# Kernel optimization log

Hardware: AMD Instinct MI355X
Metric: run time of the kernel (lower is better)

## Reference

```python
import jax, jax.numpy as jnp
from jax import lax
import numpy as np

NPOINT, RADIUS, NSAMPLE = 2048, 0.2, 32
EPS = 1e-5


def fps(xyz, npoint):
    # furthest point sampling; xyz [B,N,3] -> idx [B,npoint] int32
    B, N, _ = xyz.shape

    def body(carry, _):
        dist, far = carry  # dist [B,N], far [B]
        centroid = jnp.take_along_axis(xyz, far[:, None, None], axis=1)  # [B,1,3]
        d = jnp.sum((xyz - centroid) ** 2, -1)  # [B,N]
        dist = jnp.minimum(dist, d)
        nxt = jnp.argmax(dist, -1).astype(jnp.int32)
        return (dist, nxt), far

    init = (jnp.full((B, N), 1e10, xyz.dtype), jnp.zeros((B,), jnp.int32))
    _, idx = lax.scan(body, init, None, length=npoint)
    return jnp.transpose(idx)  # [B, npoint]


def ball_query(radius, nsample, xyz, new_xyz):
    # xyz [B,N,3], new_xyz [B,S,3] -> idx [B,S,nsample] int32
    B, N, _ = xyz.shape
    sqr = jnp.sum((new_xyz[:, :, None, :] - xyz[:, None, :, :]) ** 2, -1)  # [B,S,N]
    idx = jnp.broadcast_to(jnp.arange(N, dtype=jnp.int32), sqr.shape)
    idx = jnp.where(sqr > radius * radius, N, idx)
    idx = jnp.sort(idx, -1)[:, :, :nsample]  # first nsample in-ball indices
    first = idx[:, :, :1]
    return jnp.where(idx == N, first, idx)  # pad misses with first hit


def group(x, idx):
    # x [B,N,C], idx [B,S,K] -> [B,S,K,C]
    return jax.vmap(lambda xb, ib: xb[ib])(x, idx)


def setup_inputs() -> dict:
    key = jax.random.key(0)
    ks = jax.random.split(key, 8)
    B, N = 8, 8192
    mlp, in_c = [32, 32, 64], 6
    inp = {
        'xyz': jax.random.normal(ks[0], (B, N, 3), jnp.float32),
        'points': jax.random.normal(ks[1], (B, N, 3), jnp.float32),
    }
    cin = in_c
    for i, cout in enumerate(mlp):
        inp[f'w{i}'] = jax.random.normal(ks[2 + i], (cout, cin), jnp.float32) * (1.0 / np.sqrt(cin))
        inp[f'b{i}'] = jnp.zeros((cout,), jnp.float32)
        inp[f'g{i}'] = jnp.ones((cout,), jnp.float32)
        inp[f'be{i}'] = jnp.zeros((cout,), jnp.float32)
        cin = cout
    return inp


def reference(xyz, points, w0, b0, g0, be0, w1, b1, g1, be1, w2, b2, g2, be2):
    fps_idx = fps(xyz, NPOINT)
    new_xyz = jax.vmap(lambda xb, ib: xb[ib])(xyz, fps_idx)  # [B,S,3]
    idx = ball_query(RADIUS, NSAMPLE, xyz, new_xyz)  # [B,S,K]
    grouped_xyz = group(xyz, idx) - new_xyz[:, :, None, :]  # [B,S,K,3]
    feat = jnp.concatenate([grouped_xyz, group(points, idx)], -1)  # [B,S,K,6]
    for w, b, g, be in ((w0, b0, g0, be0), (w1, b1, g1, be1), (w2, b2, g2, be2)):
        feat = jnp.einsum('bskc,oc->bsko', feat, w) + b  # 1x1 conv
        mean = jnp.mean(feat, axis=(0, 1, 2))
        var = jnp.var(feat, axis=(0, 1, 2))
        feat = (feat - mean) * lax.rsqrt(var + EPS) * g + be  # BN (train stats)
        feat = jax.nn.relu(feat)
    new_points = jnp.max(feat, axis=2)  # max over neighborhood -> [B,S,64]
    return new_xyz, new_points
```

## Files before the change

### kernel.cpp

```cpp
#include <hip/hip_runtime.h>
#include <math.h>

#define BB 8
#define NN 8192
#define SS 2048
#define KK 32
#define NP (BB*SS*KK)
#define EPSF 1e-5f

typedef float v2f __attribute__((ext_vector_type(2)));

template <int CTRL>
__device__ __forceinline__ unsigned long long dpp_max_step(unsigned long long key) {
    unsigned lo = (unsigned)key, hi = (unsigned)(key >> 32);
    unsigned nlo = (unsigned)__builtin_amdgcn_update_dpp((int)lo, (int)lo, CTRL, 0xf, 0xf, false);
    unsigned nhi = (unsigned)__builtin_amdgcn_update_dpp((int)hi, (int)hi, CTRL, 0xf, 0xf, false);
    unsigned long long nk = ((unsigned long long)nhi << 32) | nlo;
    return nk > key ? nk : key;
}

__device__ __forceinline__ unsigned long long wave_max_u64(unsigned long long key) {
    key = dpp_max_step<0x111>(key);
    key = dpp_max_step<0x112>(key);
    key = dpp_max_step<0x114>(key);
    key = dpp_max_step<0x118>(key);
    key = dpp_max_step<0x142>(key);
    key = dpp_max_step<0x143>(key);
    return key;
}

__global__ __launch_bounds__(512) void fps_kernel(const float* __restrict__ xyz,
                                                  float* __restrict__ out_newxyz) {
#pragma clang fp contract(off)
    const int T = 512;
    const int NPAIR = 8;
    int b = blockIdx.x;
    int t = threadIdx.x;
    int wid  = t >> 6;
    int lane = t & 63;
    const float* x = xyz + b * NN * 3;
    float* nout = out_newxyz + b * SS * 3;

    __shared__ float4 lxyz[NN];
    __shared__ unsigned long long skey[2][8];

    v2f px2[NPAIR], py2[NPAIR], pz2[NPAIR], d2[NPAIR];
#pragma unroll
    for (int j = 0; j < NPAIR; j++) {
        int p0 = t + (2 * j) * T;
        int p1 = p0 + T;
        float ax = x[p0 * 3 + 0], ay = x[p0 * 3 + 1], az = x[p0 * 3 + 2];
        float bx = x[p1 * 3 + 0], by = x[p1 * 3 + 1], bz = x[p1 * 3 + 2];
        px2[j].x = ax; px2[j].y = bx;
        py2[j].x = ay; py2[j].y = by;
        pz2[j].x = az; pz2[j].y = bz;
        lxyz[p0] = make_float4(ax, ay, az, 0.f);
        lxyz[p1] = make_float4(bx, by, bz, 0.f);
        d2[j].x = 1e10f; d2[j].y = 1e10f;
    }
    __syncthreads();
    float4 c0 = lxyz[0];
    float cx = c0.x, cy = c0.y, cz = c0.z;

    for (int it = 0; it < SS; it++) {
        if (t == 0) {
            nout[it * 3 + 0] = cx;
            nout[it * 3 + 1] = cy;
            nout[it * 3 + 2] = cz;
        }
        v2f cxx, cyy, czz;
        cxx.x = cx; cxx.y = cx;
        cyy.x = cy; cyy.y = cy;
        czz.x = cz; czz.y = cz;
        float lmax = -1.0f;
        int   li   = 0;
#pragma unroll
        for (int j = 0; j < NPAIR; j++) {
            v2f dx = px2[j] - cxx;
            v2f dy = py2[j] - cyy;
            v2f dz = pz2[j] - czz;
            v2f sx = dx * dx;
            v2f sy = dy * dy;
            v2f sz = dz * dz;
            v2f ss = (sx + sy) + sz;
            float e0 = fminf(d2[j].x, ss.x);
            float e1 = fminf(d2[j].y, ss.y);
            d2[j].x = e0;
            d2[j].y = e1;
            bool g0 = e0 > lmax;
            lmax = g0 ? e0 : lmax;
            li   = g0 ? (2 * j) : li;
            bool g1 = e1 > lmax;
            lmax = g1 ? e1 : lmax;
            li   = g1 ? (2 * j + 1) : li;
        }
        int p = t + (li << 9);
        unsigned long long key =
            ((unsigned long long)__float_as_uint(lmax) << 32) | (unsigned)(~p);
        key = wave_max_u64(key);
        if (lane == 63) skey[it & 1][wid] = key;
        __syncthreads();
        unsigned long long k = skey[it & 1][0];
#pragma unroll
        for (int j = 1; j < 8; j++) {
            unsigned long long o = skey[it & 1][j];
            k = (o > k) ? o : k;
        }
        int gi = (int)(~(unsigned)k) & (NN - 1);
        float4 c = lxyz[gi];
        cx = c.x; cy = c.y; cz = c.z;
    }
}

__global__ __launch_bounds__(256) void ballq_kernel(const float* __restrict__ xyz,
                                                    const float* __restrict__ new_xyz,
                                                    int* __restrict__ idx_out) {
    int q    = blockIdx.x * 4 + (threadIdx.x >> 6);
    int lane = threadIdx.x & 63;
    int b    = q >> 11;
    const float* x = xyz + b * NN * 3;
    const float* c = new_xyz + q * 3;
    float cx = c[0], cy = c[1], cz = c[2];
    int* out = idx_out + q * KK;
    const float R2 = (float)(0.2 * 0.2);

    int count = 0;
    int first = -1;
    for (int base = 0; base < NN; base += 64) {
        int p = base + lane;
        float dx = __fsub_rn(x[p * 3 + 0], cx);
        float dy = __fsub_rn(x[p * 3 + 1], cy);
        float dz = __fsub_rn(x[p * 3 + 2], cz);
        float d  = __fadd_rn(__fadd_rn(__fmul_rn(dx, dx), __fmul_rn(dy, dy)),
                             __fmul_rn(dz, dz));
        bool in = !(d > R2);
        unsigned long long m = __ballot(in);
        if (first < 0 && m != 0ull) first = base + __ffsll((unsigned long long)m) - 1;
        int pre = __popcll(m & ((1ull << lane) - 1ull));
        int pos = count + pre;
        if (in && pos < KK) out[pos] = p;
        count += __popcll(m);
        if (count >= KK) break;
    }
    for (int i2 = count + lane; i2 < KK; i2 += 64) out[i2] = first;
}

__device__ __forceinline__ void load_in6(const float* __restrict__ xyz,
                                         const float* __restrict__ points,
                                         const float* __restrict__ new_xyz,
                                         const int* __restrict__ idx, int p, float inx[6]) {
    int bs = p >> 5;
    int b  = bs >> 11;
    int pt = idx[p];
    const float* xb = xyz + ((long)b * NN + pt) * 3;
    const float* pb = points + ((long)b * NN + pt) * 3;
    const float* nx = new_xyz + bs * 3;
    inx[0] = xb[0] - nx[0];
    inx[1] = xb[1] - nx[1];
    inx[2] = xb[2] - nx[2];
    inx[3] = pb[0];
    inx[4] = pb[1];
    inx[5] = pb[2];
}

template <int CIN, int COUT>
__device__ __forceinline__ void linear(const float* __restrict__ w,
                                       const float* __restrict__ bias,
                                       const float* xin, float* yout) {
#pragma unroll
    for (int o = 0; o < COUT; o++) {
        float acc = bias[o];
#pragma unroll
        for (int j = 0; j < CIN; j++) acc = fmaf(w[o * CIN + j], xin[j], acc);
        yout[o] = acc;
    }
}

template <int C>
__device__ __forceinline__ void bn_coef(const float* __restrict__ stats,
                                        const float* __restrict__ g,
                                        const float* __restrict__ be,
                                        float* s_sc, float* s_sh) {
    int t = threadIdx.x;
    if (t < C) {
        float mean = stats[t] * (1.0f / (float)NP);
        float var  = stats[C + t] * (1.0f / (float)NP) - mean * mean;
        float rstd = 1.0f / sqrtf(var + EPSF);
        float sc = g[t] * rstd;
        s_sc[t] = sc;
        s_sh[t] = be[t] - mean * sc;
    }
    __syncthreads();
}

template <int C>
__device__ __forceinline__ void accum_stats(const float* y, float* __restrict__ gstats) {
    __shared__ float buf[256][33];
    int t = threadIdx.x;
#pragma unroll
    for (int h = 0; h < C / 32; h++) {
        __syncthreads();
#pragma unroll
        for (int c = 0; c < 32; c++) buf[t][c] = y[h * 32 + c];
        __syncthreads();
        if (t < 32) {
            float s = 0.f, sq = 0.f;
            for (int r = 0; r < 256; r++) {
                float v = buf[r][t];
                s += v;
                sq = fmaf(v, v, sq);
            }
            atomicAdd(&gstats[h * 32 + t], s);
            atomicAdd(&gstats[C + h * 32 + t], sq);
        }
    }
}

__global__ __launch_bounds__(256) void l0_stats_kernel(
    const float* __restrict__ xyz, const float* __restrict__ points,
    const float* __restrict__ new_xyz, const int* __restrict__ idx,
    const float* __restrict__ w0, const float* __restrict__ b0_,
    float* __restrict__ stats0) {
    int p = blockIdx.x * 256 + threadIdx.x;
    float inx[6];
    load_in6(xyz, points, new_xyz, idx, p, inx);
    float y0[32];
    linear<6, 32>(w0, b0_, inx, y0);
    accum_stats<32>(y0, stats0);
}

__global__ __launch_bounds__(256) void l1_stats_kernel(
    const float* __restrict__ xyz, const float* __restrict__ points,
    const float* __restrict__ new_xyz, const int* __restrict__ idx,
    const float* __restrict__ w0, const float* __restrict__ b0_,
    const float* __restrict__ g0, const float* __restrict__ be0,
    const float* __restrict__ w1, const float* __restrict__ b1_,
    const float* __restrict__ stats0, float* __restrict__ stats1) {
    __shared__ float sc0[32], sh0[32];
    bn_coef<32>(stats0, g0, be0, sc0, sh0);
    int p = blockIdx.x * 256 + threadIdx.x;
    float inx[6];
    load_in6(xyz, points, new_xyz, idx, p, inx);
    float y0[32];
    linear<6, 32>(w0, b0_, inx, y0);
#pragma unroll
    for (int c = 0; c < 32; c++) y0[c] = fmaxf(fmaf(y0[c], sc0[c], sh0[c]), 0.f);
    float y1[32];
    linear<32, 32>(w1, b1_, y0, y1);
    accum_stats<32>(y1, stats1);
}

__global__ __launch_bounds__(256) void l2_stats_kernel(
    const float* __restrict__ xyz, const float* __restrict__ points,
    const float* __restrict__ new_xyz, const int* __restrict__ idx,
    const float* __restrict__ w0, const float* __restrict__ b0_,
    const float* __restrict__ g0, const float* __restrict__ be0,
    const float* __restrict__ w1, const float* __restrict__ b1_,
    const float* __restrict__ g1, const float* __restrict__ be1,
    const float* __restrict__ w2, const float* __restrict__ b2_,
    const float* __restrict__ stats0, const float* __restrict__ stats1,
    float* __restrict__ stats2) {
    __shared__ float sc0[32], sh0[32], sc1[32], sh1[32];
    bn_coef<32>(stats0, g0, be0, sc0, sh0);
    bn_coef<32>(stats1, g1, be1, sc1, sh1);
    int p = blockIdx.x * 256 + threadIdx.x;
    float inx[6];
    load_in6(xyz, points, new_xyz, idx, p, inx);
    float y0[32];
    linear<6, 32>(w0, b0_, inx, y0);
#pragma unroll
    for (int c = 0; c < 32; c++) y0[c] = fmaxf(fmaf(y0[c], sc0[c], sh0[c]), 0.f);
    float y1[32];
    linear<32, 32>(w1, b1_, y0, y1);
#pragma unroll
    for (int c = 0; c < 32; c++) y1[c] = fmaxf(fmaf(y1[c], sc1[c], sh1[c]), 0.f);
    float y2[64];
    linear<32, 64>(w2, b2_, y1, y2);
    accum_stats<64>(y2, stats2);
}

__global__ __launch_bounds__(256) void final_kernel(
    const float* __restrict__ xyz, const float* __restrict__ points,
    const float* __restrict__ new_xyz, const int* __restrict__ idx,
    const float* __restrict__ w0, const float* __restrict__ b0_,
    const float* __restrict__ g0, const float* __restrict__ be0,
    const float* __restrict__ w1, const float* __restrict__ b1_,
    const float* __restrict__ g1, const float* __restrict__ be1,
    const float* __restrict__ w2, const float* __restrict__ b2_,
    const float* __restrict__ g2, const float* __restrict__ be2,
    const float* __restrict__ stats0, const float* __restrict__ stats1,
    const float* __restrict__ stats2, float* __restrict__ out_points) {
    __shared__ float sc0[32], sh0[32], sc1[32], sh1[32], sc2[64], sh2[64];
    bn_coef<32>(stats0, g0, be0, sc0, sh0);
    bn_coef<32>(stats1, g1, be1, sc1, sh1);
    bn_coef<64>(stats2, g2, be2, sc2, sh2);
    int p = blockIdx.x * 256 + threadIdx.x;
    float inx[6];
    load_in6(xyz, points, new_xyz, idx, p, inx);
    float y0[32];
    linear<6, 32>(w0, b0_, inx, y0);
#pragma unroll
    for (int c = 0; c < 32; c++) y0[c] = fmaxf(fmaf(y0[c], sc0[c], sh0[c]), 0.f);
    float y1[32];
    linear<32, 32>(w1, b1_, y0, y1);
#pragma unroll
    for (int c = 0; c < 32; c++) y1[c] = fmaxf(fmaf(y1[c], sc1[c], sh1[c]), 0.f);
    float y2[64];
    linear<32, 64>(w2, b2_, y1, y2);
#pragma unroll
    for (int c = 0; c < 64; c++) {
        float v = fmaxf(fmaf(y2[c], sc2[c], sh2[c]), 0.f);
#pragma unroll
        for (int off = 1; off < 32; off <<= 1)
            v = fmaxf(v, __shfl_xor(v, off));
        y2[c] = v;
    }
    int lane = threadIdx.x & 63;
    if ((lane & 31) == 0) {
        int bs = p >> 5;
        float4* o = (float4*)(out_points + (long)bs * 64);
#pragma unroll
        for (int c4 = 0; c4 < 16; c4++)
            o[c4] = make_float4(y2[c4 * 4], y2[c4 * 4 + 1], y2[c4 * 4 + 2], y2[c4 * 4 + 3]);
    }
}

extern "C" void kernel_launch(void* const* d_in, const int* in_sizes, int n_in,
                              void* d_out, int out_size, void* d_ws, size_t ws_size,
                              hipStream_t stream) {
    (void)in_sizes; (void)n_in; (void)out_size; (void)ws_size;
    const float* xyz    = (const float*)d_in[0];
    const float* points = (const float*)d_in[1];
    const float* w0  = (const float*)d_in[2];
    const float* b0_ = (const float*)d_in[3];
    const float* g0  = (const float*)d_in[4];
    const float* be0 = (const float*)d_in[5];
    const float* w1  = (const float*)d_in[6];
    const float* b1_ = (const float*)d_in[7];
    const float* g1  = (const float*)d_in[8];
    const float* be1 = (const float*)d_in[9];
    const float* w2  = (const float*)d_in[10];
    const float* b2_ = (const float*)d_in[11];
    const float* g2  = (const float*)d_in[12];
    const float* be2 = (const float*)d_in[13];

    float* out        = (float*)d_out;
    float* out_newxyz = out;
    float* out_points = out + BB * SS * 3;

    int*   idx    = (int*)d_ws;
    float* stats  = (float*)d_ws + NP;
    float* stats0 = stats;
    float* stats1 = stats + 64;
    float* stats2 = stats + 128;

    hipMemsetAsync(stats, 0, 256 * sizeof(float), stream);

    fps_kernel<<<BB, 512, 0, stream>>>(xyz, out_newxyz);
    ballq_kernel<<<BB * SS / 4, 256, 0, stream>>>(xyz, out_newxyz, idx);
    l0_stats_kernel<<<NP / 256, 256, 0, stream>>>(xyz, points, out_newxyz, idx, w0, b0_, stats0);
    l1_stats_kernel<<<NP / 256, 256, 0, stream>>>(xyz, points, out_newxyz, idx,
                                                  w0, b0_, g0, be0, w1, b1_, stats0, stats1);
    l2_stats_kernel<<<NP / 256, 256, 0, stream>>>(xyz, points, out_newxyz, idx,
                                                  w0, b0_, g0, be0, w1, b1_, g1, be1,
                                                  w2, b2_, stats0, stats1, stats2);
    final_kernel<<<NP / 256, 256, 0, stream>>>(xyz, points, out_newxyz, idx,
                                               w0, b0_, g0, be0, w1, b1_, g1, be1,
                                               w2, b2_, g2, be2, stats0, stats1, stats2,
                                               out_points);
}
```

Baseline: 2.346 ms.

## Split FPS per batch across four cooperating blocks with global-memory argmax exchange

Furthest point sampling now uses four blocks per batch instead of one, each owning a quarter of the points. Every iteration the blocks publish their local max key to global memory, spin on per-block sequence counters, and then reduce the four keys. The aim is to use more CUs for the serial FPS loop, which previously ran on only 8 blocks. The cost is a cross-block global-memory handshake on each of the 2048 iterations, which adds latency and needs a cooperative launch to guarantee co-residency.

```diff
diff --git a/kernel.cpp b/kernel.cpp
--- a/kernel.cpp
+++ b/kernel.cpp
@@ -7,6 +7,7 @@
 #define KK 32
 #define NP (BB*SS*KK)
 #define EPSF 1e-5f
+#define FG 4
 
 typedef float v2f __attribute__((ext_vector_type(2)));
 
@@ -30,40 +31,50 @@
 }
 
 __global__ __launch_bounds__(512) void fps_kernel(const float* __restrict__ xyz,
-                                                  float* __restrict__ out_newxyz) {
+                                                  float* __restrict__ out_newxyz,
+                                                  unsigned long long* __restrict__ comm,
+                                                  unsigned* __restrict__ seqp) {
 #pragma clang fp contract(off)
     const int T = 512;
-    const int NPAIR = 8;
-    int b = blockIdx.x;
+    const int NPAIR = 2;
+    int blk = blockIdx.x;
+    int b = blk >> 2;
+    int g = blk & (FG - 1);
     int t = threadIdx.x;
     int wid  = t >> 6;
     int lane = t & 63;
     const float* x = xyz + b * NN * 3;
     float* nout = out_newxyz + b * SS * 3;
+    int base = g * (NN / FG);
+    int slot = b * FG + g;
 
     __shared__ float4 lxyz[NN];
     __shared__ unsigned long long skey[2][8];
+    __shared__ unsigned long long gkey[2][FG];
+
+#pragma unroll
+    for (int i = 0; i < NN / T; i++) {
+        int p = t + i * T;
+        lxyz[p] = make_float4(x[p * 3 + 0], x[p * 3 + 1], x[p * 3 + 2], 0.f);
+    }
+    __syncthreads();
 
     v2f px2[NPAIR], py2[NPAIR], pz2[NPAIR], d2[NPAIR];
 #pragma unroll
     for (int j = 0; j < NPAIR; j++) {
-        int p0 = t + (2 * j) * T;
+        int p0 = base + t + (2 * j) * T;
         int p1 = p0 + T;
-        float ax = x[p0 * 3 + 0], ay = x[p0 * 3 + 1], az = x[p0 * 3 + 2];
-        float bx = x[p1 * 3 + 0], by = x[p1 * 3 + 1], bz = x[p1 * 3 + 2];
-        px2[j].x = ax; px2[j].y = bx;
-        py2[j].x = ay; py2[j].y = by;
-        pz2[j].x = az; pz2[j].y = bz;
-        lxyz[p0] = make_float4(ax, ay, az, 0.f);
-        lxyz[p1] = make_float4(bx, by, bz, 0.f);
+        float4 a = lxyz[p0], c = lxyz[p1];
+        px2[j].x = a.x; px2[j].y = c.x;
+        py2[j].x = a.y; py2[j].y = c.y;
+        pz2[j].x = a.z; pz2[j].y = c.z;
         d2[j].x = 1e10f; d2[j].y = 1e10f;
     }
-    __syncthreads();
     float4 c0 = lxyz[0];
     float cx = c0.x, cy = c0.y, cz = c0.z;
 
     for (int it = 0; it < SS; it++) {
-        if (t == 0) {
+        if (g == 0 && t == 0) {
             nout[it * 3 + 0] = cx;
             nout[it * 3 + 1] = cy;
             nout[it * 3 + 2] = cz;
@@ -94,16 +105,36 @@
             lmax = g1 ? e1 : lmax;
             li   = g1 ? (2 * j + 1) : li;
         }
-        int p = t + (li << 9);
+        int p = base + t + (li << 9);
         unsigned long long key =
             ((unsigned long long)__float_as_uint(lmax) << 32) | (unsigned)(~p);
         key = wave_max_u64(key);
         if (lane == 63) skey[it & 1][wid] = key;
         __syncthreads();
-        unsigned long long k = skey[it & 1][0];
-#pragma unroll
-        for (int j = 1; j < 8; j++) {
-            unsigned long long o = skey[it & 1][j];
+        if (t == 0) {
+            unsigned long long kb = skey[it & 1][0];
+#pragma unroll
+            for (int j = 1; j < 8; j++) {
+                unsigned long long o = skey[it & 1][j];
+                kb = (o > kb) ? o : kb;
+            }
+            __hip_atomic_store(&comm[(it & 1) * (BB * FG) + slot], kb,
+                               __ATOMIC_RELAXED, __HIP_MEMORY_SCOPE_AGENT);
+            __hip_atomic_store(&seqp[slot], (unsigned)(it + 1),
+                               __ATOMIC_RELEASE, __HIP_MEMORY_SCOPE_AGENT);
+        }
+        if (t < FG) {
+            int s = b * FG + t;
+            while (__hip_atomic_load(&seqp[s], __ATOMIC_ACQUIRE,
+                                     __HIP_MEMORY_SCOPE_AGENT) < (unsigned)(it + 1)) {}
+            gkey[it & 1][t] = __hip_atomic_load(&comm[(it & 1) * (BB * FG) + s],
+                                                __ATOMIC_RELAXED, __HIP_MEMORY_SCOPE_AGENT);
+        }
+        __syncthreads();
+        unsigned long long k = gkey[it & 1][0];
+#pragma unroll
+        for (int j = 1; j < FG; j++) {
+            unsigned long long o = gkey[it & 1][j];
             k = (o > k) ? o : k;
         }
         int gi = (int)(~(unsigned)k) & (NN - 1);
@@ -353,10 +384,16 @@
     float* stats0 = stats;
     float* stats1 = stats + 64;
     float* stats2 = stats + 128;
-
-    hipMemsetAsync(stats, 0, 256 * sizeof(float), stream);
-
-    fps_kernel<<<BB, 512, 0, stream>>>(xyz, out_newxyz);
+    unsigned long long* comm = (unsigned long long*)((char*)d_ws + (size_t)NP * 4 + 1024);
+    unsigned* seqp = (unsigned*)(comm + 2 * BB * FG);
+
+    hipMemsetAsync(stats, 0, 1024 + 512 + 128, stream);
+
+    {
+        void* args[] = { (void*)&xyz, (void*)&out_newxyz, (void*)&comm, (void*)&seqp };
+        hipLaunchCooperativeKernel((const void*)fps_kernel, dim3(BB * FG), dim3(512),
+                                   args, 0, stream);
+    }
     ballq_kernel<<<BB * SS / 4, 256, 0, stream>>>(xyz, out_newxyz, idx);
     l0_stats_kernel<<<NP / 256, 256, 0, stream>>>(xyz, points, out_newxyz, idx, w0, b0_, stats0);
     l1_stats_kernel<<<NP / 256, 256, 0, stream>>>(xyz, points, out_newxyz, idx,
```

After: 5.849 ms. 149% more time.
